# Performance work log

Hardware: AMD Instinct MI355X
Metric: run time of the kernel (lower is better)

## Reference

```python
import jax, jax.numpy as jnp
import numpy as np

N = 50000        # bs * n_node
E = 800000       # n_edge
INPUT_NF = 64
HIDDEN_NF = 64
N_CHANNEL = 4
D = 3            # spatial dim
EDGE_D = 16
EPS = 1e-12      # F.normalize clamp


def _unif(k, shape, fan_in):
    s = 1.0 / np.sqrt(fan_in)
    return jax.random.uniform(k, shape, jnp.float32, -s, s)


def setup_inputs() -> dict:
    key = jax.random.key(0)
    ks = jax.random.split(key, 12)
    h = jax.random.normal(ks[0], (N, INPUT_NF), jnp.float32)
    coord = jax.random.normal(ks[1], (N, N_CHANNEL, D), jnp.float32)
    row = jax.random.randint(ks[2], (E,), 0, N)
    col = jax.random.randint(ks[3], (E,), 0, N)
    edge_attr = jax.random.normal(ks[4], (E, EDGE_D), jnp.float32)
    kv_in = INPUT_NF + N_CHANNEL * N_CHANNEL + EDGE_D
    Wq = _unif(ks[5], (INPUT_NF, HIDDEN_NF), INPUT_NF)
    bq = _unif(ks[6], (HIDDEN_NF,), INPUT_NF)
    Wkv = _unif(ks[7], (kv_in, 2 * HIDDEN_NF), kv_in)
    bkv = _unif(ks[8], (2 * HIDDEN_NF,), kv_in)
    W1 = _unif(ks[9], (HIDDEN_NF, HIDDEN_NF), HIDDEN_NF)
    b1 = _unif(ks[10], (HIDDEN_NF,), HIDDEN_NF)
    # xavier_uniform with gain=0.001, no bias
    lim = 0.001 * np.sqrt(6.0 / (HIDDEN_NF + N_CHANNEL))
    W2 = jax.random.uniform(ks[11], (HIDDEN_NF, N_CHANNEL), jnp.float32, -lim, lim)
    return dict(h=h, coord=coord, row=row, col=col, edge_attr=edge_attr,
                Wq=Wq, bq=bq, Wkv=Wkv, bkv=bkv, W1=W1, b1=b1, W2=W2)


def reference(h, coord, edge_attr, Wq, bq, Wkv, bkv, W1, b1, W2, row, col):
    n_node = h.shape[0]
    # coord2radial
    coord_diff = coord[row] - coord[col]                                # [E,C,D]
    radial = jnp.einsum('ecd,efd->ecf', coord_diff, coord_diff)         # [E,C,C]
    # F.normalize(radial, dim=0): L2-normalize across the edge dimension
    norm = jnp.maximum(jnp.sqrt(jnp.sum(radial * radial, axis=0, keepdims=True)), EPS)
    radial = radial / norm
    # att_model
    q = h[row] @ Wq + bq                                                # [E,H]
    target_feat = jnp.concatenate(
        [radial.reshape(radial.shape[0], -1), h[col], edge_attr], axis=1)
    kv = target_feat @ Wkv + bkv                                        # [E,2H]
    k, v = kv[:, 0::2], kv[:, 1::2]                                     # [E,H] each
    alpha = jnp.sum(q * k, axis=1)                                      # [E]
    # scatter_softmax over segments given by row (numerically stable)
    seg_max = jax.ops.segment_max(alpha, row, num_segments=n_node)
    ex = jnp.exp(alpha - seg_max[row])
    seg_sum = jax.ops.segment_sum(ex, row, num_segments=n_node)
    att = ex / seg_sum[row]                                             # [E]
    # node_model (dropout in eval mode = identity)
    h_out = h + jax.ops.segment_sum(att[:, None] * v, row, num_segments=n_node)
    # coord_model: coord_mlp = Linear -> SiLU -> Linear(no bias)
    coord_v = att[:, None] * (jax.nn.silu(v @ W1 + b1) @ W2)            # [E,C]
    trans = coord_diff * coord_v[:, :, None]                            # [E,C,D]
    coord_out = coord + jax.ops.segment_sum(trans, row, num_segments=n_node)
    return h_out, coord_out, att
```

## Files before the change

kernel.cpp:

```cpp
#include <hip/hip_runtime.h>
#include <math.h>

#define NN 50000
#define NE 800000
#define NPREB 1024

typedef __attribute__((ext_vector_type(8))) short short8;
typedef __attribute__((ext_vector_type(4))) float floatx4;

__device__ __forceinline__ unsigned short bf16_of(float x) {
  unsigned u = __float_as_uint(x);
  u += 0x7fffu + ((u >> 16) & 1u);
  return (unsigned short)(u >> 16);
}
__device__ __forceinline__ float bf2f(unsigned short u) {
  return __uint_as_float(((unsigned)u) << 16);
}
__device__ __forceinline__ unsigned pack_bf(float a, float b) {
  unsigned ua = __float_as_uint(a); ua += 0x7fffu + ((ua >> 16) & 1u);
  unsigned ub = __float_as_uint(b); ub += 0x7fffu + ((ub >> 16) & 1u);
  return (ua >> 16) | (ub & 0xffff0000u);
}
__device__ __forceinline__ float blo(unsigned w) { return __uint_as_float(w << 16); }
__device__ __forceinline__ float bhi(unsigned w) { return __uint_as_float(w & 0xffff0000u); }

__global__ __launch_bounds__(256)
void k_pre(const float* __restrict__ coord, const int* __restrict__ row,
           const int* __restrict__ col, const float* __restrict__ Wkv,
           const float* __restrict__ W1, const float* __restrict__ Wq,
           float* __restrict__ norm_part, int* __restrict__ deg,
           unsigned short* __restrict__ Bkvb, unsigned short* __restrict__ W1tb,
           unsigned* __restrict__ Wqp) {
  __shared__ float nred[4][16];
  const int gid = blockIdx.x * 256 + threadIdx.x;
  const int np = gridDim.x * 256;
  for (int idx = gid; idx < 128 * 96; idx += np) {
    int n = idx & 127, kk = idx >> 7;
    float w = (n < 64) ? Wkv[kk * 128 + 2 * n] : Wkv[kk * 128 + 2 * (n - 64) + 1];
    Bkvb[n * 104 + kk] = bf16_of(w);
  }
  for (int idx = gid; idx < 64 * 64; idx += np) {
    int n = idx & 63, kk = idx >> 6;
    W1tb[n * 88 + kk] = bf16_of(W1[kk * 64 + n]);
  }
  for (int idx = gid; idx < 32 * 64; idx += np) {
    int i2 = idx >> 6, j = idx & 63;
    Wqp[idx] = pack_bf(Wq[(2 * i2) * 64 + j], Wq[(2 * i2 + 1) * 64 + j]);
  }
  const int lane = threadIdx.x & 63;
  const int grp = lane >> 4, g = lane & 15;
  const int c4 = g >> 2, f4 = g & 3;
  const int wid = blockIdx.x * 4 + (threadIdx.x >> 6);
  const int nw = gridDim.x * 4;
  float acc = 0.f;
  for (int base = wid * 4; base < NE; base += nw * 4) {
    int e = base + grp;
    int r = row[e], c = col[e];
    float cd = 0.f;
    if (g < 12) cd = coord[r * 12 + g] - coord[c * 12 + g];
    float rad = 0.f;
#pragma unroll
    for (int d = 0; d < 3; ++d)
      rad += __shfl(cd, grp * 16 + c4 * 3 + d) * __shfl(cd, grp * 16 + f4 * 3 + d);
    acc += rad * rad;
    if (g == 0) atomicAdd(deg + r, 1);
  }
  acc += __shfl_xor(acc, 16);
  acc += __shfl_xor(acc, 32);
  if (lane < 16) nred[threadIdx.x >> 6][lane] = acc;
  __syncthreads();
  if (threadIdx.x < 16) {
    float s = nred[0][threadIdx.x] + nred[1][threadIdx.x] +
              nred[2][threadIdx.x] + nred[3][threadIdx.x];
    norm_part[blockIdx.x * 16 + threadIdx.x] = s;
  }
}

__global__ __launch_bounds__(1024)
void k_scanq(const int* __restrict__ deg, int* __restrict__ startA,
             int* __restrict__ cursor, const float* __restrict__ norm_part,
             float* __restrict__ rnorm, const float* __restrict__ h,
             const unsigned* __restrict__ Wqp, const float* __restrict__ bq,
             unsigned short* __restrict__ qg2, unsigned short* __restrict__ hb) {
  __shared__ int part[1024];
  __shared__ float nr[64][16];
  __shared__ unsigned sWqp[32 * 64];
  __shared__ float sHr[16][64];
  const int t = threadIdx.x;
  if (blockIdx.x == 0) {
    {
      const int i = t >> 4, c = t & 15;
      float s = 0.f;
#pragma unroll
      for (int j = 0; j < 16; ++j) s += norm_part[((i + 64 * j) << 4) + c];
      nr[i][c] = s;
    }
    __syncthreads();
    if (t < 16) {
      float s = 0.f;
#pragma unroll 8
      for (int i = 0; i < 64; ++i) s += nr[i][t];
      rnorm[t] = 1.0f / fmaxf(sqrtf(s), 1e-12f);
    }
    const int CH = (NN + 1023) / 1024;
    const int lo = t * CH, hi = (lo + CH < NN) ? lo + CH : NN;
    int s = 0;
    for (int i = lo; i < hi; ++i) s += deg[i];
    part[t] = s;
    __syncthreads();
    for (int off = 1; off < 1024; off <<= 1) {
      int v = (t >= off) ? part[t - off] : 0;
      __syncthreads();
      part[t] += v;
      __syncthreads();
    }
    int base = (t == 0) ? 0 : part[t - 1];
    for (int i = lo; i < hi; ++i) {
      startA[i] = base; cursor[i] = base; base += deg[i];
    }
    if (t == 1023) startA[NN] = base;
    return;
  }
  for (int idx = t; idx < 2048; idx += 1024) sWqp[idx] = Wqp[idx];
  __syncthreads();
  const int wv = t >> 6, lane = t & 63;
  const int node = (blockIdx.x - 1) * 16 + wv;
  float hv = h[(size_t)node * 64 + lane];
  sHr[wv][lane] = hv;
  hb[(size_t)node * 64 + lane] = bf16_of(hv);
  float q = bq[lane];
  const float2* hp = (const float2*)sHr[wv];
#pragma unroll 8
  for (int i2 = 0; i2 < 32; ++i2) {
    unsigned w = sWqp[i2 * 64 + lane];
    float2 hbv = hp[i2];
    q += hbv.x * blo(w) + hbv.y * bhi(w);
  }
  qg2[(size_t)node * 64 + (lane & 15) * 4 + (lane >> 4)] = bf16_of(q);
}

__global__ void k_scatter(const int* __restrict__ row, int* __restrict__ cursor,
                          int* __restrict__ eperm, int* __restrict__ iperm) {
  int e = blockIdx.x * 256 + threadIdx.x;
  if (e < NE) {
    int p = atomicAdd(cursor + row[e], 1);
    eperm[p] = e;
    iperm[e] = p;
  }
}

__global__ __launch_bounds__(512, 4)
void k_kv(const unsigned short* __restrict__ hb, const float* __restrict__ coord,
          const int* __restrict__ row, const int* __restrict__ col,
          const float* __restrict__ edge_attr, const float* __restrict__ bkv,
          const float* __restrict__ b1, const float* __restrict__ W2,
          const float* __restrict__ rnorm, const int* __restrict__ eperm,
          const unsigned short* __restrict__ Bkvb,
          const unsigned short* __restrict__ W1tb,
          const unsigned short* __restrict__ qg2,
          float* __restrict__ exg, float* __restrict__ l_g,
          float* __restrict__ hacc_g, float* __restrict__ cacc_g) {
  __shared__ __align__(16) unsigned short sA[128][104];
  __shared__ __align__(16) unsigned short sB[128][104];
  __shared__ __align__(16) unsigned short sW1t[64][88];
  __shared__ unsigned short cdb[128][12];
  __shared__ int sCol[128], sRow[128], sE[128];

  const int tid = threadIdx.x;
  const int base = blockIdx.x * 128;

  if (tid < 128) {
    int e = eperm[base + tid];
    sE[tid] = e; sCol[tid] = col[e]; sRow[tid] = row[e];
  }
  {
    const uint4* gb = (const uint4*)Bkvb;
    uint4* sb = (uint4*)&sB[0][0];
    for (int idx = tid; idx < 1664; idx += 512) sb[idx] = gb[idx];
    const uint4* gw = (const uint4*)W1tb;
    uint4* sw = (uint4*)&sW1t[0][0];
    for (int idx = tid; idx < 704; idx += 512) sw[idx] = gw[idx];
  }
  __syncthreads();

  for (int idx = tid; idx < 1024; idx += 512) {
    int s = idx >> 3, q8 = idx & 7;
    uint4 u = ((const uint4*)(hb + (size_t)sCol[s] * 64))[q8];
    *(uint4*)&sA[s][16 + q8 * 8] = u;
  }
  for (int idx = tid; idx < 1024; idx += 512) {
    int s = idx >> 3, c2 = idx & 7;
    float2 ea = ((const float2*)(edge_attr + (size_t)sE[s] * 16))[c2];
    *(unsigned*)&sA[s][80 + 2 * c2] = pack_bf(ea.x, ea.y);
  }
  {
    const int wv = tid >> 6, lane = tid & 63;
    const int grp = lane >> 4, g = lane & 15;
    const int c4 = g >> 2, f4 = g & 3;
    const float rn = rnorm[g];
#pragma unroll
    for (int it = 0; it < 4; ++it) {
      int slot = 16 * wv + it * 4 + grp;
      int r = sRow[slot], c = sCol[slot];
      float cd = 0.f;
      if (g < 12) cd = coord[r * 12 + g] - coord[c * 12 + g];
      float rad = 0.f;
#pragma unroll
      for (int d = 0; d < 3; ++d)
        rad += __shfl(cd, grp * 16 + c4 * 3 + d) * __shfl(cd, grp * 16 + f4 * 3 + d);
      sA[slot][g] = bf16_of(rad * rn);
      if (g < 12) cdb[slot][g] = bf16_of(cd);
    }
  }
  __syncthreads();

  const int wv = tid >> 6, lane = tid & 63;
  const int m16 = lane & 15, quad = lane >> 4;
  const int arow = 16 * wv + m16;

  floatx4 acc[8];
#pragma unroll
  for (int i = 0; i < 8; ++i) acc[i] = (floatx4){0.f, 0.f, 0.f, 0.f};
#pragma unroll
  for (int ks = 0; ks < 3; ++ks) {
    short8 af = *(const short8*)&sA[arow][ks * 32 + quad * 8];
#pragma unroll
    for (int nt = 0; nt < 8; ++nt) {
      short8 bf = *(const short8*)&sB[nt * 16 + m16][ks * 32 + quad * 8];
      acc[nt] = __builtin_amdgcn_mfma_f32_16x16x32_bf16(af, bf, acc[nt], 0, 0, 0);
    }
  }
#pragma unroll
  for (int nt = 0; nt < 4; ++nt) {
    float bk = bkv[2 * (m16 + 16 * nt)];
    float bv = bkv[2 * (m16 + 16 * nt) + 1];
#pragma unroll
    for (int r = 0; r < 4; ++r) { acc[nt][r] += bk; acc[nt + 4][r] += bv; }
  }
  float part[4] = {0.f, 0.f, 0.f, 0.f};
#pragma unroll
  for (int r = 0; r < 4; ++r) {
    int nrow = sRow[16 * wv + quad * 4 + r];
    uint2 qp = *(const uint2*)(qg2 + (size_t)nrow * 64 + m16 * 4);
    part[r] += blo(qp.x) * acc[0][r] + bhi(qp.x) * acc[1][r] +
               blo(qp.y) * acc[2][r] + bhi(qp.y) * acc[3][r];
  }
#pragma unroll
  for (int off = 1; off < 16; off <<= 1) {
#pragma unroll
    for (int r = 0; r < 4; ++r) part[r] += __shfl_xor(part[r], off);
  }
  float ex[4];
#pragma unroll
  for (int r = 0; r < 4; ++r) ex[r] = __expf(part[r]);
  if (m16 == 0) {
#pragma unroll
    for (int r = 0; r < 4; ++r)
      exg[base + 16 * wv + quad * 4 + r] = ex[r];
  }
#pragma unroll
  for (int nt = 0; nt < 4; ++nt)
#pragma unroll
    for (int r = 0; r < 4; ++r)
      sA[16 * wv + quad * 4 + r][m16 + 16 * nt] = bf16_of(acc[4 + nt][r]);
  floatx4 tacc[4];
#pragma unroll
  for (int i = 0; i < 4; ++i) tacc[i] = (floatx4){0.f, 0.f, 0.f, 0.f};
#pragma unroll
  for (int ks = 0; ks < 2; ++ks) {
    short8 af = *(const short8*)&sA[arow][ks * 32 + quad * 8];
#pragma unroll
    for (int nt = 0; nt < 4; ++nt) {
      short8 bf = *(const short8*)&sW1t[nt * 16 + m16][ks * 32 + quad * 8];
      tacc[nt] = __builtin_amdgcn_mfma_f32_16x16x32_bf16(af, bf, tacc[nt], 0, 0, 0);
    }
  }
#pragma unroll
  for (int nt = 0; nt < 4; ++nt) {
    float bb = b1[m16 + 16 * nt];
#pragma unroll
    for (int r = 0; r < 4; ++r) {
      float t = tacc[nt][r] + bb;
      tacc[nt][r] = t / (1.f + __expf(-t));
    }
  }
  float cvp[4][4];
#pragma unroll
  for (int r = 0; r < 4; ++r)
#pragma unroll
    for (int c = 0; c < 4; ++c) cvp[r][c] = 0.f;
#pragma unroll
  for (int nt = 0; nt < 4; ++nt) {
    float4 w2r = ((const float4*)W2)[m16 + 16 * nt];
#pragma unroll
    for (int r = 0; r < 4; ++r) {
      cvp[r][0] += tacc[nt][r] * w2r.x;
      cvp[r][1] += tacc[nt][r] * w2r.y;
      cvp[r][2] += tacc[nt][r] * w2r.z;
      cvp[r][3] += tacc[nt][r] * w2r.w;
    }
  }
#pragma unroll
  for (int off = 1; off < 16; off <<= 1) {
#pragma unroll
    for (int r = 0; r < 4; ++r)
#pragma unroll
      for (int c = 0; c < 4; ++c) cvp[r][c] += __shfl_xor(cvp[r][c], off);
  }
  float tr[4];
#pragma unroll
  for (int r = 0; r < 4; ++r) {
    if (m16 < 12) {
      float cvv = (m16 < 3) ? cvp[r][0] : (m16 < 6) ? cvp[r][1]
                : (m16 < 9) ? cvp[r][2] : cvp[r][3];
      tr[r] = bf2f(cdb[16 * wv + quad * 4 + r][m16]) * cvv;
    } else tr[r] = 0.f;
  }

  int s = 0;
  while (s < 16) {
    int n = sRow[16 * wv + s];
    int e2 = s + 1;
    while (e2 < 16 && sRow[16 * wv + e2] == n) ++e2;
    float hp0 = 0.f, hp1 = 0.f, hp2 = 0.f, hp3 = 0.f, lp = 0.f, cp = 0.f;
#pragma unroll
    for (int r = 0; r < 4; ++r) {
      int rowi = quad * 4 + r;
      float w = (rowi >= s && rowi < e2) ? ex[r] : 0.f;
      hp0 += w * acc[4][r];
      hp1 += w * acc[5][r];
      hp2 += w * acc[6][r];
      hp3 += w * acc[7][r];
      lp  += (rowi >= s && rowi < e2) ? ex[r] : 0.f;
      cp  += w * tr[r];
    }
    hp0 += __shfl_xor(hp0, 16); hp0 += __shfl_xor(hp0, 32);
    hp1 += __shfl_xor(hp1, 16); hp1 += __shfl_xor(hp1, 32);
    hp2 += __shfl_xor(hp2, 16); hp2 += __shfl_xor(hp2, 32);
    hp3 += __shfl_xor(hp3, 16); hp3 += __shfl_xor(hp3, 32);
    lp  += __shfl_xor(lp, 16);  lp  += __shfl_xor(lp, 32);
    cp  += __shfl_xor(cp, 16);  cp  += __shfl_xor(cp, 32);
    if (quad == 0) {
      float* hg = hacc_g + (size_t)n * 64;
      atomicAdd(hg + m16,      hp0);
      atomicAdd(hg + m16 + 16, hp1);
      atomicAdd(hg + m16 + 32, hp2);
      atomicAdd(hg + m16 + 48, hp3);
      if (m16 < 12) atomicAdd(cacc_g + (size_t)n * 12 + m16, cp);
      if (m16 == 0) atomicAdd(l_g + n, lp);
    }
    s = e2;
  }
}

__global__ __launch_bounds__(256)
void k_fin(const float* __restrict__ h, const float* __restrict__ coord,
           const int* __restrict__ row, const int* __restrict__ iperm,
           const float* __restrict__ exg, const float* __restrict__ l_g,
           const float* __restrict__ hacc_g, const float* __restrict__ cacc_g,
           float* __restrict__ out) {
  const int wv = threadIdx.x >> 6, lane = threadIdx.x & 63;
  const int node = blockIdx.x * 4 + wv;
  const float l = l_g[node];
  const float inv = (l > 0.f) ? 1.f / l : 0.f;
  out[node * 64 + lane] =
      h[(size_t)node * 64 + lane] + hacc_g[(size_t)node * 64 + lane] * inv;
  if (lane < 12)
    out[NN * 64 + node * 12 + lane] =
        coord[node * 12 + lane] + cacc_g[(size_t)node * 12 + lane] * inv;
  const int e = blockIdx.x * 256 + threadIdx.x;
  if (e < NE) {
    float le = l_g[row[e]];
    out[NN * 64 + NN * 12 + e] = exg[iperm[e]] / le;
  }
}

extern "C" void kernel_launch(void* const* d_in, const int* in_sizes, int n_in,
                              void* d_out, int out_size, void* d_ws, size_t ws_size,
                              hipStream_t stream) {
  const float* h         = (const float*)d_in[0];
  const float* coord     = (const float*)d_in[1];
  const int*   row       = (const int*)d_in[2];
  const int*   col       = (const int*)d_in[3];
  const float* edge_attr = (const float*)d_in[4];
  const float* Wq        = (const float*)d_in[5];
  const float* bq        = (const float*)d_in[6];
  const float* Wkv       = (const float*)d_in[7];
  const float* bkv       = (const float*)d_in[8];
  const float* W1        = (const float*)d_in[9];
  const float* b1        = (const float*)d_in[10];
  const float* W2        = (const float*)d_in[11];
  float* out = (float*)d_out;

  size_t off = 0;
  char* wsb = (char*)d_ws;
  auto alloc = [&](size_t bytes) {
    off = (off + 255) & ~(size_t)255;
    void* p = wsb + off; off += bytes; return p;
  };
  int*            deg      = (int*)alloc((size_t)NN * 4);
  float*          l_g      = (float*)alloc((size_t)NN * 4);
  float*          hacc_g   = (float*)alloc((size_t)NN * 64 * 4);
  float*          cacc_g   = (float*)alloc((size_t)NN * 12 * 4);
  size_t zbytes = off;
  float*          norm_part= (float*)alloc((size_t)NPREB * 16 * 4);
  float*          rnorm    = (float*)alloc(16 * 4);
  int*            startA   = (int*)alloc(((size_t)NN + 1) * 4);
  int*            cursor   = (int*)alloc((size_t)NN * 4);
  int*            eperm    = (int*)alloc((size_t)NE * 4);
  int*            iperm    = (int*)alloc((size_t)NE * 4);
  float*          exg      = (float*)alloc((size_t)NE * 4);
  unsigned short* qg2      = (unsigned short*)alloc((size_t)NN * 64 * 2);
  unsigned short* hb       = (unsigned short*)alloc((size_t)NN * 64 * 2);
  unsigned short* Bkvb     = (unsigned short*)alloc(128 * 104 * 2);
  unsigned short* W1tb     = (unsigned short*)alloc(64 * 88 * 2);
  unsigned*       Wqp      = (unsigned*)alloc(32 * 64 * 4);

  hipMemsetAsync(d_ws, 0, zbytes, stream);

  k_pre<<<NPREB, 256, 0, stream>>>(coord, row, col, Wkv, W1, Wq,
                                   norm_part, deg, Bkvb, W1tb, Wqp);
  k_scanq<<<1 + NN / 16, 1024, 0, stream>>>(deg, startA, cursor, norm_part,
                                            rnorm, h, Wqp, bq, qg2, hb);
  k_scatter<<<(NE + 255) / 256, 256, 0, stream>>>(row, cursor, eperm, iperm);
  k_kv<<<NE / 128, 512, 0, stream>>>(hb, coord, row, col, edge_attr, bkv, b1, W2,
                                     rnorm, eperm, Bkvb, W1tb, qg2,
                                     exg, l_g, hacc_g, cacc_g);
  k_fin<<<NN / 4, 256, 0, stream>>>(h, coord, row, iperm, exg, l_g,
                                    hacc_g, cacc_g, out);
}
```

Measured before the change: 533.4 us.

## Shrink k_kv LDS footprint and swizzle blocks across XCDs

Cuts shared memory in k_kv by packing row/col into one 32-bit array, reusing sB for W1t after the first GEMM, and storing coord diffs in spare sA columns. W1t is prefetched into registers and written to LDS behind an extra barrier. Launch bounds are raised to 6 blocks per CU, and block indices are remapped so each XCD processes a contiguous range of edges, improving L2 locality. The costs are extra barriers, more register pressure, and an edge_attr index reload from global eperm; packing row and col into 16 bits each limits node ids to 65535, which holds for N=50000.

```diff
diff --git a/kernel.cpp b/kernel.cpp
--- a/kernel.cpp
+++ b/kernel.cpp
@@ -149,7 +149,7 @@
   }
 }
 
-__global__ __launch_bounds__(512, 4)
+__global__ __launch_bounds__(512, 6)
 void k_kv(const unsigned short* __restrict__ hb, const float* __restrict__ coord,
           const int* __restrict__ row, const int* __restrict__ col,
           const float* __restrict__ edge_attr, const float* __restrict__ bkv,
@@ -162,59 +162,67 @@
           float* __restrict__ hacc_g, float* __restrict__ cacc_g) {
   __shared__ __align__(16) unsigned short sA[128][104];
   __shared__ __align__(16) unsigned short sB[128][104];
-  __shared__ __align__(16) unsigned short sW1t[64][88];
-  __shared__ unsigned short cdb[128][12];
-  __shared__ int sCol[128], sRow[128], sE[128];
+  __shared__ unsigned sRC[128];
+  unsigned short (*sW1t)[88] = (unsigned short (*)[88])&sB[0][0];
 
   const int tid = threadIdx.x;
-  const int base = blockIdx.x * 128;
+  const int nwg = gridDim.x;
+  const int qq = nwg >> 3, rr = nwg & 7;
+  const int xcd = blockIdx.x & 7, loc = blockIdx.x >> 3;
+  const int bswz = (xcd < rr ? xcd * (qq + 1) : rr * (qq + 1) + (xcd - rr) * qq) + loc;
+  const int base = bswz * 128;
+
+  const uint4* gw = (const uint4*)W1tb;
+  uint4 w1a = gw[tid];
+  uint4 w1b;
+  if (tid < 192) w1b = gw[512 + tid];
 
   if (tid < 128) {
     int e = eperm[base + tid];
-    sE[tid] = e; sCol[tid] = col[e]; sRow[tid] = row[e];
+    sRC[tid] = ((unsigned)row[e] << 16) | (unsigned)col[e];
   }
   {
     const uint4* gb = (const uint4*)Bkvb;
     uint4* sb = (uint4*)&sB[0][0];
     for (int idx = tid; idx < 1664; idx += 512) sb[idx] = gb[idx];
-    const uint4* gw = (const uint4*)W1tb;
-    uint4* sw = (uint4*)&sW1t[0][0];
-    for (int idx = tid; idx < 704; idx += 512) sw[idx] = gw[idx];
   }
   __syncthreads();
 
   for (int idx = tid; idx < 1024; idx += 512) {
-    int s = idx >> 3, q8 = idx & 7;
-    uint4 u = ((const uint4*)(hb + (size_t)sCol[s] * 64))[q8];
-    *(uint4*)&sA[s][16 + q8 * 8] = u;
+    int s = idx >> 3, k8 = idx & 7;
+    unsigned c = sRC[s] & 0xffffu;
+    uint4 u = ((const uint4*)(hb + (size_t)c * 64))[k8];
+    *(uint4*)&sA[s][16 + k8 * 8] = u;
   }
   for (int idx = tid; idx < 1024; idx += 512) {
     int s = idx >> 3, c2 = idx & 7;
-    float2 ea = ((const float2*)(edge_attr + (size_t)sE[s] * 16))[c2];
+    int e = eperm[base + s];
+    float2 ea = ((const float2*)(edge_attr + (size_t)e * 16))[c2];
     *(unsigned*)&sA[s][80 + 2 * c2] = pack_bf(ea.x, ea.y);
   }
+  const int wv = tid >> 6, lane = tid & 63;
+  float cdp[4];
   {
-    const int wv = tid >> 6, lane = tid & 63;
     const int grp = lane >> 4, g = lane & 15;
     const int c4 = g >> 2, f4 = g & 3;
     const float rn = rnorm[g];
 #pragma unroll
     for (int it = 0; it < 4; ++it) {
       int slot = 16 * wv + it * 4 + grp;
-      int r = sRow[slot], c = sCol[slot];
+      unsigned rc = sRC[slot];
+      int r = (int)(rc >> 16), c = (int)(rc & 0xffffu);
       float cd = 0.f;
       if (g < 12) cd = coord[r * 12 + g] - coord[c * 12 + g];
+      cdp[it] = cd;
       float rad = 0.f;
 #pragma unroll
       for (int d = 0; d < 3; ++d)
         rad += __shfl(cd, grp * 16 + c4 * 3 + d) * __shfl(cd, grp * 16 + f4 * 3 + d);
       sA[slot][g] = bf16_of(rad * rn);
-      if (g < 12) cdb[slot][g] = bf16_of(cd);
-    }
-  }
-  __syncthreads();
-
-  const int wv = tid >> 6, lane = tid & 63;
+    }
+  }
+  __syncthreads();
+
   const int m16 = lane & 15, quad = lane >> 4;
   const int arow = 16 * wv + m16;
 
@@ -240,7 +248,7 @@
   float part[4] = {0.f, 0.f, 0.f, 0.f};
 #pragma unroll
   for (int r = 0; r < 4; ++r) {
-    int nrow = sRow[16 * wv + quad * 4 + r];
+    unsigned nrow = sRC[16 * wv + quad * 4 + r] >> 16;
     uint2 qp = *(const uint2*)(qg2 + (size_t)nrow * 64 + m16 * 4);
     part[r] += blo(qp.x) * acc[0][r] + bhi(qp.x) * acc[1][r] +
                blo(qp.y) * acc[2][r] + bhi(qp.y) * acc[3][r];
@@ -263,6 +271,18 @@
 #pragma unroll
     for (int r = 0; r < 4; ++r)
       sA[16 * wv + quad * 4 + r][m16 + 16 * nt] = bf16_of(acc[4 + nt][r]);
+#pragma unroll
+  for (int it = 0; it < 4; ++it)
+    if (m16 < 12) sA[16 * wv + it * 4 + quad][64 + m16] = bf16_of(cdp[it]);
+
+  __syncthreads();
+  {
+    unsigned short* sw = &sB[0][0];
+    *(uint4*)&sw[(size_t)tid * 8] = w1a;
+    if (tid < 192) *(uint4*)&sw[(size_t)(512 + tid) * 8] = w1b;
+  }
+  __syncthreads();
+
   floatx4 tacc[4];
 #pragma unroll
   for (int i = 0; i < 4; ++i) tacc[i] = (floatx4){0.f, 0.f, 0.f, 0.f};
@@ -313,15 +333,15 @@
     if (m16 < 12) {
       float cvv = (m16 < 3) ? cvp[r][0] : (m16 < 6) ? cvp[r][1]
                 : (m16 < 9) ? cvp[r][2] : cvp[r][3];
-      tr[r] = bf2f(cdb[16 * wv + quad * 4 + r][m16]) * cvv;
+      tr[r] = bf2f(sA[16 * wv + quad * 4 + r][64 + m16]) * cvv;
     } else tr[r] = 0.f;
   }
 
   int s = 0;
   while (s < 16) {
-    int n = sRow[16 * wv + s];
+    int n = (int)(sRC[16 * wv + s] >> 16);
     int e2 = s + 1;
-    while (e2 < 16 && sRow[16 * wv + e2] == n) ++e2;
+    while (e2 < 16 && (int)(sRC[16 * wv + e2] >> 16) == n) ++e2;
     float hp0 = 0.f, hp1 = 0.f, hp2 = 0.f, hp3 = 0.f, lp = 0.f, cp = 0.f;
 #pragma unroll
     for (int r = 0; r < 4; ++r) {
```

Result: slower. 550.3 us (+3.2%).
